# Optimization experiments

Measured on AMD Instinct MI355X. Metric: run time of the kernel, lower is better.

## Reference

```python
import jax, jax.numpy as jnp
import numpy as np

IN_FEATURES = 1024
OUT_FEATURES = 256
GRID_SIZE = 5
SPLINE_ORDER = 3
SCALE_BASE = 1.0
GRID_RANGE = (-1.0, 1.0)


def make_grid():
    h = (GRID_RANGE[1] - GRID_RANGE[0]) / GRID_SIZE
    g = jnp.arange(-SPLINE_ORDER, GRID_SIZE + SPLINE_ORDER + 1, dtype=jnp.float32) * h + GRID_RANGE[0]
    # (in_features, grid_size + 2*spline_order + 1) = (1024, 12)
    return jnp.broadcast_to(g[None, :], (IN_FEATURES, g.shape[0]))


def setup_inputs() -> dict:
    key = jax.random.key(0)
    k1, k2, k3 = jax.random.split(key, 3)
    batch = 16384
    x = jax.random.normal(k1, (batch, IN_FEATURES), dtype=jnp.float32)
    base_weight = jax.random.normal(k2, (OUT_FEATURES, IN_FEATURES), dtype=jnp.float32) * 0.03
    n_basis = GRID_SIZE + SPLINE_ORDER  # 8
    spline_weight = (jax.random.uniform(k3, (OUT_FEATURES, IN_FEATURES * n_basis), dtype=jnp.float32) - 0.5) * 0.1 / n_basis
    grid = make_grid()
    return {"x": x, "base_weight": base_weight, "spline_weight": spline_weight, "grid": grid}


def b_splines(x, grid):
    # x: (B, F) -> (B, F, grid_size + spline_order)
    xe = x[:, :, None]  # (B, F, 1)
    bases = ((xe >= grid[:, :-1]) & (xe < grid[:, 1:])).astype(x.dtype)
    for k in range(1, SPLINE_ORDER + 1):
        left = (xe - grid[:, : -(k + 1)]) / (grid[:, k:-1] - grid[:, : -(k + 1)])
        right = (grid[:, k + 1 :] - xe) / (grid[:, k + 1 :] - grid[:, 1:-k])
        bases = left * bases[:, :, :-1] + right * bases[:, :, 1:]
    return bases.reshape(x.shape[0], -1)  # (B, F*(grid_size+spline_order))


def reference(x, base_weight, spline_weight, grid):
    base_out = jax.nn.silu(x) @ (base_weight * SCALE_BASE).T  # (B, out)
    spline_basis = b_splines(x, grid)                          # (B, F*8)
    spline_out = spline_basis @ spline_weight.T                # (B, out)
    return base_out + spline_out
```

## Files before the change

### kernel.cpp

```cpp
#include <hip/hip_runtime.h>
#include <cstdint>
#include <cstddef>

typedef unsigned short u16;
typedef unsigned int   u32;
typedef unsigned long long u64;
typedef __attribute__((ext_vector_type(8))) short short8;
typedef __attribute__((ext_vector_type(4))) float f32x4;

#define M_ROWS 16384
#define N_COLS 256
#define IN_F   1024
#define K_SPL  8192
#define K_TOT  9216
#define NCHUNK 144
#define SPLITK 2
#define CPB    (NCHUNK / SPLITK)

__device__ __forceinline__ u32 f2bf1(float f) {
  u32 u = __float_as_uint(f);
  u += 0x7fffu + ((u >> 16) & 1u);
  return u >> 16;
}
__device__ __forceinline__ u32 pk2(float a, float b) {
  return f2bf1(a) | (f2bf1(b) << 16);
}
__device__ __forceinline__ float silu(float v) {
  return v * __builtin_amdgcn_rcpf(1.f + __expf(-v));
}

__device__ __forceinline__ uint4 basis8(float xv) {
  float u = fmaf(xv, 2.5f, 5.5f);
  int i0 = (int)u;
  float fr = u - (float)i0;
  float fr2 = fr * fr, fr3 = fr2 * fr;
  float om  = 1.f - fr;
  float om3 = om * om * om;
  float w0 = om3 * (1.f / 6.f);
  float w3 = fr3 * (1.f / 6.f);
  float w1 = fmaf(fr3, 0.5f, fmaf(fr2, -1.f, 2.f / 3.f));
  float w2 = fmaf(fr + fr2 - fr3, 0.5f, 1.f / 6.f);
  u64 W = (u64)pk2(w0, w1) | ((u64)pk2(w2, w3) << 32);
  if (!(u >= 0.f && u < 11.f)) W = 0ull;
  int s = (i0 - 3) * 16;
  u64 lo, hi;
  if (s >= 64)      { int r = s - 64; lo = 0ull; hi = (r < 64) ? (W << r) : 0ull; }
  else if (s > 0)   { lo = W << s;    hi = W >> (64 - s); }
  else if (s == 0)  { lo = W;         hi = 0ull; }
  else              { int r = -s;     lo = (r < 64) ? (W >> r) : 0ull; hi = 0ull; }
  uint4 o;
  o.x = (u32)lo; o.y = (u32)(lo >> 32); o.z = (u32)hi; o.w = (u32)(hi >> 32);
  return o;
}

__global__ void pack_weights(const float* __restrict__ bw, const float* __restrict__ sw,
                             u16* __restrict__ Bp, float* __restrict__ out) {
  int o  = blockIdx.y;
  int k4 = (blockIdx.x * blockDim.x + threadIdx.x) * 4;
  const float* src = (k4 < K_SPL) ? (sw + (size_t)o * K_SPL + k4)
                                  : (bw + (size_t)o * IN_F + (k4 - K_SPL));
  float a = src[0], b = src[1], c = src[2], d = src[3];
  uint2 v; v.x = pk2(a, b); v.y = pk2(c, d);
  *(uint2*)(Bp + (size_t)o * K_TOT + k4) = v;

  int flat = (blockIdx.y * gridDim.x + blockIdx.x) * blockDim.x + threadIdx.x;
  if (flat < (M_ROWS * N_COLS / 8)) {
    float4 z = {0.f, 0.f, 0.f, 0.f};
    ((float4*)out)[flat * 2]     = z;
    ((float4*)out)[flat * 2 + 1] = z;
  }
}

__global__ __launch_bounds__(256, 2)
void kan_gemm(const float* __restrict__ x, const u16* __restrict__ Bp,
              float* __restrict__ out) {
  __shared__ __align__(16) u16 As[2][64 * 64];
  __shared__ __align__(16) u16 Bs[2][256 * 64];

  const int tid  = threadIdx.x;
  const int lane = tid & 63;
  const int w    = tid >> 6;

  const int bid  = blockIdx.x;
  const int kid  = bid & 1;
  const int mb   = bid >> 1;
  const int row0 = mb * 64;
  const int cs   = kid * CPB, c1 = cs + CPB;

  f32x4 acc[4][4];
#pragma unroll
  for (int i = 0; i < 4; ++i)
#pragma unroll
    for (int j = 0; j < 4; ++j)
      acc[i][j] = (f32x4){0.f, 0.f, 0.f, 0.f};

  const int sr = tid >> 2;
  const int sq = tid & 3;

  const int lm = lane & 15;
  const int kg = lane >> 4;
  int a_off[2][4], b_off[2][4];
#pragma unroll
  for (int h = 0; h < 2; ++h) {
    int c = h * 4 + kg;
#pragma unroll
    for (int i = 0; i < 4; ++i) {
      int ra = i * 16 + lm;
      a_off[h][i] = ra * 64 + ((c ^ (ra & 7)) * 8);
    }
#pragma unroll
    for (int j = 0; j < 4; ++j) {
      int rb = w * 64 + j * 16 + lm;
      b_off[h][j] = rb * 64 + ((c ^ (rb & 7)) * 8);
    }
  }

  float px0, px1;
  float4 pb0, pb1, pb2, pb3;

  auto LOADX = [&](int c) {
    if (c < 128) {
      const float* xp = x + (size_t)(row0 + sr) * IN_F + c * 8 + sq;
      px0 = xp[0];
      px1 = xp[4];
    } else {
      const float* xp = x + (size_t)(row0 + sr) * IN_F + (c - 128) * 64 + sq * 16;
      pb0 = *(const float4*)xp;
      pb1 = *(const float4*)(xp + 4);
      pb2 = *(const float4*)(xp + 8);
      pb3 = *(const float4*)(xp + 12);
    }
  };

  auto BUILD = [&](int c, u16* A) {
    if (c < 128) {
      *(uint4*)(A + sr * 64 + ((sq ^ (sr & 7)) * 8))       = basis8(px0);
      *(uint4*)(A + sr * 64 + (((sq + 4) ^ (sr & 7)) * 8)) = basis8(px1);
    } else {
      uint4 q0, q1;
      q0.x = pk2(silu(pb0.x), silu(pb0.y));
      q0.y = pk2(silu(pb0.z), silu(pb0.w));
      q0.z = pk2(silu(pb1.x), silu(pb1.y));
      q0.w = pk2(silu(pb1.z), silu(pb1.w));
      q1.x = pk2(silu(pb2.x), silu(pb2.y));
      q1.y = pk2(silu(pb2.z), silu(pb2.w));
      q1.z = pk2(silu(pb3.x), silu(pb3.y));
      q1.w = pk2(silu(pb3.z), silu(pb3.w));
      int cc0 = sq * 2, cc1 = sq * 2 + 1;
      *(uint4*)(A + sr * 64 + ((cc0 ^ (sr & 7)) * 8)) = q0;
      *(uint4*)(A + sr * 64 + ((cc1 ^ (sr & 7)) * 8)) = q1;
    }
  };

  auto STAGEB = [&](int c, u16* B) {
#pragma unroll
    for (int it = 0; it < 8; ++it) {
      int s = tid + it * 256;
      int r_ = s >> 3, cc = (s & 7) ^ (r_ & 7);
      const u16* gp = Bp + (size_t)r_ * K_TOT + c * 64 + cc * 8;
      __builtin_amdgcn_global_load_lds((const __attribute__((address_space(1))) void*)gp,
                                       (__attribute__((address_space(3))) void*)(B + s * 8),
                                       16, 0, 0);
    }
  };

  LOADX(cs);
  BUILD(cs, As[0]);
  STAGEB(cs, Bs[0]);
  LOADX(cs + 1);
  __syncthreads();

  int b = 0;
  for (int c = cs; c < c1; ++c) {
    if (c + 1 < c1) {
      STAGEB(c + 1, Bs[b ^ 1]);
      BUILD(c + 1, As[b ^ 1]);
      if (c + 2 < c1) LOADX(c + 2);
    }
    const u16* Ab = As[b];
    const u16* Bb = Bs[b];
#pragma unroll
    for (int h = 0; h < 2; ++h) {
      short8 af[4], bf[4];
#pragma unroll
      for (int i = 0; i < 4; ++i) af[i] = *(const short8*)(Ab + a_off[h][i]);
#pragma unroll
      for (int j = 0; j < 4; ++j) bf[j] = *(const short8*)(Bb + b_off[h][j]);
#pragma unroll
      for (int i = 0; i < 4; ++i)
#pragma unroll
        for (int j = 0; j < 4; ++j)
          acc[i][j] = __builtin_amdgcn_mfma_f32_16x16x32_bf16(af[i], bf[j], acc[i][j], 0, 0, 0);
    }
    __syncthreads();
    b ^= 1;
  }

  const int lc = lane & 15;
  const int lr = (lane >> 4) * 4;
#pragma unroll
  for (int i = 0; i < 4; ++i) {
#pragma unroll
    for (int j = 0; j < 4; ++j) {
      int gr = row0 + i * 16 + lr;
      int gc = w * 64 + j * 16 + lc;
      float* po = out + (size_t)gr * N_COLS + gc;
#pragma unroll
      for (int r = 0; r < 4; ++r)
        unsafeAtomicAdd(po + (size_t)r * N_COLS, acc[i][j][r]);
    }
  }
}

extern "C" void kernel_launch(void* const* d_in, const int* in_sizes, int n_in,
                              void* d_out, int out_size, void* d_ws, size_t ws_size,
                              hipStream_t stream) {
  const float* x  = (const float*)d_in[0];
  const float* bw = (const float*)d_in[1];
  const float* sw = (const float*)d_in[2];
  float* out = (float*)d_out;
  u16* Bp = (u16*)d_ws;

  dim3 pgrid(K_TOT / 4 / 256, N_COLS);
  pack_weights<<<pgrid, 256, 0, stream>>>(bw, sw, Bp, out);

  kan_gemm<<<M_ROWS / 64 * SPLITK, 256, 0, stream>>>(x, Bp, out);
}
```

Before: 214.7 us.

## Drop LDS double buffering and raise split-K to three for occupancy

Shared memory drops from two buffers to a single A and B stage, which roughly halves LDS per block. Launch bounds rise to three blocks per CU and the K dimension is split three ways, giving more blocks and more waves in flight. In exchange, loading the B tile and building the basis functions no longer overlap with the MFMA work inside a block, since each chunk now waits on a barrier before compute. A third atomic-add pass on the output is also added.

Result: no change. 216.7 us (+1.0%).

```diff
diff --git a/kernel.cpp b/kernel.cpp
--- a/kernel.cpp
+++ b/kernel.cpp
@@ -14,7 +14,7 @@
 #define K_SPL  8192
 #define K_TOT  9216
 #define NCHUNK 144
-#define SPLITK 2
+#define SPLITK 3
 #define CPB    (NCHUNK / SPLITK)
 
 __device__ __forceinline__ u32 f2bf1(float f) {
@@ -71,19 +71,19 @@
   }
 }
 
-__global__ __launch_bounds__(256, 2)
+__global__ __launch_bounds__(256, 3)
 void kan_gemm(const float* __restrict__ x, const u16* __restrict__ Bp,
               float* __restrict__ out) {
-  __shared__ __align__(16) u16 As[2][64 * 64];
-  __shared__ __align__(16) u16 Bs[2][256 * 64];
+  __shared__ __align__(16) u16 As[64 * 64];
+  __shared__ __align__(16) u16 Bs[256 * 64];
 
   const int tid  = threadIdx.x;
   const int lane = tid & 63;
   const int w    = tid >> 6;
 
   const int bid  = blockIdx.x;
-  const int kid  = bid & 1;
-  const int mb   = bid >> 1;
+  const int mb   = bid / 3;
+  const int kid  = bid - mb * 3;
   const int row0 = mb * 64;
   const int cs   = kid * CPB, c1 = cs + CPB;
 
@@ -132,10 +132,10 @@
     }
   };
 
-  auto BUILD = [&](int c, u16* A) {
+  auto BUILD = [&](int c) {
     if (c < 128) {
-      *(uint4*)(A + sr * 64 + ((sq ^ (sr & 7)) * 8))       = basis8(px0);
-      *(uint4*)(A + sr * 64 + (((sq + 4) ^ (sr & 7)) * 8)) = basis8(px1);
+      *(uint4*)(As + sr * 64 + ((sq ^ (sr & 7)) * 8))       = basis8(px0);
+      *(uint4*)(As + sr * 64 + (((sq + 4) ^ (sr & 7)) * 8)) = basis8(px1);
     } else {
       uint4 q0, q1;
       q0.x = pk2(silu(pb0.x), silu(pb0.y));
@@ -147,45 +147,36 @@
       q1.z = pk2(silu(pb3.x), silu(pb3.y));
       q1.w = pk2(silu(pb3.z), silu(pb3.w));
       int cc0 = sq * 2, cc1 = sq * 2 + 1;
-      *(uint4*)(A + sr * 64 + ((cc0 ^ (sr & 7)) * 8)) = q0;
-      *(uint4*)(A + sr * 64 + ((cc1 ^ (sr & 7)) * 8)) = q1;
+      *(uint4*)(As + sr * 64 + ((cc0 ^ (sr & 7)) * 8)) = q0;
+      *(uint4*)(As + sr * 64 + ((cc1 ^ (sr & 7)) * 8)) = q1;
     }
   };
 
-  auto STAGEB = [&](int c, u16* B) {
+  auto STAGEB = [&](int c) {
 #pragma unroll
     for (int it = 0; it < 8; ++it) {
       int s = tid + it * 256;
       int r_ = s >> 3, cc = (s & 7) ^ (r_ & 7);
       const u16* gp = Bp + (size_t)r_ * K_TOT + c * 64 + cc * 8;
       __builtin_amdgcn_global_load_lds((const __attribute__((address_space(1))) void*)gp,
-                                       (__attribute__((address_space(3))) void*)(B + s * 8),
+                                       (__attribute__((address_space(3))) void*)(Bs + s * 8),
                                        16, 0, 0);
     }
   };
 
   LOADX(cs);
-  BUILD(cs, As[0]);
-  STAGEB(cs, Bs[0]);
-  LOADX(cs + 1);
-  __syncthreads();
-
-  int b = 0;
   for (int c = cs; c < c1; ++c) {
-    if (c + 1 < c1) {
-      STAGEB(c + 1, Bs[b ^ 1]);
-      BUILD(c + 1, As[b ^ 1]);
-      if (c + 2 < c1) LOADX(c + 2);
-    }
-    const u16* Ab = As[b];
-    const u16* Bb = Bs[b];
+    BUILD(c);
+    STAGEB(c);
+    __syncthreads();
+    if (c + 1 < c1) LOADX(c + 1);
 #pragma unroll
     for (int h = 0; h < 2; ++h) {
       short8 af[4], bf[4];
 #pragma unroll
-      for (int i = 0; i < 4; ++i) af[i] = *(const short8*)(Ab + a_off[h][i]);
-#pragma unroll
-      for (int j = 0; j < 4; ++j) bf[j] = *(const short8*)(Bb + b_off[h][j]);
+      for (int i = 0; i < 4; ++i) af[i] = *(const short8*)(As + a_off[h][i]);
+#pragma unroll
+      for (int j = 0; j < 4; ++j) bf[j] = *(const short8*)(Bs + b_off[h][j]);
 #pragma unroll
       for (int i = 0; i < 4; ++i)
 #pragma unroll
@@ -193,7 +184,6 @@
           acc[i][j] = __builtin_amdgcn_mfma_f32_16x16x32_bf16(af[i], bf[j], acc[i][j], 0, 0, 0);
     }
     __syncthreads();
-    b ^= 1;
   }
 
   const int lc = lane & 15;
@@ -224,5 +214,5 @@
   dim3 pgrid(K_TOT / 4 / 256, N_COLS);
   pack_weights<<<pgrid, 256, 0, stream>>>(bw, sw, Bp, out);
 
-  kan_gemm<<<M_ROWS / 64 * SPLITK, 256, 0, stream>>>(x, Bp, out);
-}
+  kan_gemm<<<(M_ROWS / 64) * SPLITK, 256, 0, stream>>>(x, Bp, out);
+}
```

## Load B fragments directly from global into registers and raise split-K to three

Applied to the files above, without the earlier changes.

Weight tiles are no longer staged through shared memory with async global-to-LDS loads. Each lane now reads its MFMA B fragments straight from global memory (L2/cache) into registers every chunk. This frees most of the shared memory, so split-K rises from 2 to 3 and launch bounds target 3 blocks per CU for more occupancy. The risk is that uncoalesced per-lane 16-byte global loads sit on the critical path with no prefetch, and the extra split adds more atomic adds to the output.

After: 267.8 us. 1.25x slower.

```diff
diff --git a/kernel.cpp b/kernel.cpp
--- a/kernel.cpp
+++ b/kernel.cpp
@@ -14,7 +14,7 @@
 #define K_SPL  8192
 #define K_TOT  9216
 #define NCHUNK 144
-#define SPLITK 2
+#define SPLITK 3
 #define CPB    (NCHUNK / SPLITK)
 
 __device__ __forceinline__ u32 f2bf1(float f) {
@@ -71,19 +71,18 @@
   }
 }
 
-__global__ __launch_bounds__(256, 2)
+__global__ __launch_bounds__(256, 3)
 void kan_gemm(const float* __restrict__ x, const u16* __restrict__ Bp,
               float* __restrict__ out) {
   __shared__ __align__(16) u16 As[2][64 * 64];
-  __shared__ __align__(16) u16 Bs[2][256 * 64];
 
   const int tid  = threadIdx.x;
   const int lane = tid & 63;
   const int w    = tid >> 6;
 
   const int bid  = blockIdx.x;
-  const int kid  = bid & 1;
-  const int mb   = bid >> 1;
+  const int mb   = bid / 3;
+  const int kid  = bid - mb * 3;
   const int row0 = mb * 64;
   const int cs   = kid * CPB, c1 = cs + CPB;
 
@@ -99,21 +98,22 @@
 
   const int lm = lane & 15;
   const int kg = lane >> 4;
-  int a_off[2][4], b_off[2][4];
+
+  int a_off[2][4];
 #pragma unroll
   for (int h = 0; h < 2; ++h) {
-    int c = h * 4 + kg;
+    int cc = h * 4 + kg;
 #pragma unroll
     for (int i = 0; i < 4; ++i) {
       int ra = i * 16 + lm;
-      a_off[h][i] = ra * 64 + ((c ^ (ra & 7)) * 8);
-    }
-#pragma unroll
-    for (int j = 0; j < 4; ++j) {
-      int rb = w * 64 + j * 16 + lm;
-      b_off[h][j] = rb * 64 + ((c ^ (rb & 7)) * 8);
-    }
-  }
+      a_off[h][i] = ra * 64 + ((cc ^ (ra & 7)) * 8);
+    }
+  }
+
+  const u16* bptr[4];
+#pragma unroll
+  for (int j = 0; j < 4; ++j)
+    bptr[j] = Bp + (size_t)(w * 64 + j * 16 + lm) * K_TOT + (size_t)cs * 64 + kg * 8;
 
   float px0, px1;
   float4 pb0, pb1, pb2, pb3;
@@ -152,45 +152,34 @@
     }
   };
 
-  auto STAGEB = [&](int c, u16* B) {
-#pragma unroll
-    for (int it = 0; it < 8; ++it) {
-      int s = tid + it * 256;
-      int r_ = s >> 3, cc = (s & 7) ^ (r_ & 7);
-      const u16* gp = Bp + (size_t)r_ * K_TOT + c * 64 + cc * 8;
-      __builtin_amdgcn_global_load_lds((const __attribute__((address_space(1))) void*)gp,
-                                       (__attribute__((address_space(3))) void*)(B + s * 8),
-                                       16, 0, 0);
-    }
-  };
-
   LOADX(cs);
   BUILD(cs, As[0]);
-  STAGEB(cs, Bs[0]);
   LOADX(cs + 1);
   __syncthreads();
 
   int b = 0;
   for (int c = cs; c < c1; ++c) {
-    if (c + 1 < c1) {
-      STAGEB(c + 1, Bs[b ^ 1]);
-      BUILD(c + 1, As[b ^ 1]);
-      if (c + 2 < c1) LOADX(c + 2);
-    }
+    short8 bf[2][4];
+#pragma unroll
+    for (int j = 0; j < 4; ++j) {
+      bf[0][j] = *(const short8*)(bptr[j]);
+      bf[1][j] = *(const short8*)(bptr[j] + 32);
+      bptr[j] += 64;
+    }
+    if (c + 1 < c1) BUILD(c + 1, As[b ^ 1]);
+    if (c + 2 < c1) LOADX(c + 2);
+
     const u16* Ab = As[b];
-    const u16* Bb = Bs[b];
 #pragma unroll
     for (int h = 0; h < 2; ++h) {
-      short8 af[4], bf[4];
+      short8 af[4];
 #pragma unroll
       for (int i = 0; i < 4; ++i) af[i] = *(const short8*)(Ab + a_off[h][i]);
 #pragma unroll
-      for (int j = 0; j < 4; ++j) bf[j] = *(const short8*)(Bb + b_off[h][j]);
-#pragma unroll
       for (int i = 0; i < 4; ++i)
 #pragma unroll
         for (int j = 0; j < 4; ++j)
-          acc[i][j] = __builtin_amdgcn_mfma_f32_16x16x32_bf16(af[i], bf[j], acc[i][j], 0, 0, 0);
+          acc[i][j] = __builtin_amdgcn_mfma_f32_16x16x32_bf16(af[i], bf[h][j], acc[i][j], 0, 0, 0);
     }
     __syncthreads();
     b ^= 1;
@@ -224,5 +213,5 @@
   dim3 pgrid(K_TOT / 4 / 256, N_COLS);
   pack_weights<<<pgrid, 256, 0, stream>>>(bw, sw, Bp, out);
 
-  kan_gemm<<<M_ROWS / 64 * SPLITK, 256, 0, stream>>>(x, Bp, out);
-}
+  kan_gemm<<<(M_ROWS / 64) * SPLITK, 256, 0, stream>>>(x, Bp, out);
+}
```
